# Optimization experiments

Hardware: AMD Instinct MI355X
Metric: run time of the kernel (lower is better)

Reference implementation:

```python
import math
import jax, jax.numpy as jnp
import numpy as np

# ---- static configuration (matches init_kwargs) ----
NM, NT, NF = 250000, 8000, 60000      # movable, terminals(fixed), filler
N = NM + NT + NF
XL = YL = ZL = 0.0
XH, YH, ZH = 512.0, 512.0, 8.0
BSX = BSY = BSZ = 1.0
NX = int(round((XH - XL) / BSX))
NY = int(round((YH - YL) / BSY))
NZ = int(round((ZH - ZL) / BSZ))
TD = 1.0                              # target density
PAD = 1
SQRT2 = 1.4142135623730951
BIN_VOL = BSX * BSY * BSZ


def _padding_mask():
    m = np.ones((NX, NY, NZ), dtype=bool)
    m[PAD:NX - PAD, PAD:NY - PAD, PAD:NZ - PAD] = False
    return jnp.asarray(m)


def _axis_overlap(p0, s, bl, bs, K, NB):
    """Overlap of segment [p0, p0+s] with K consecutive bins starting at floor bin.
    Returns bin indices [n,K], overlap lengths [n,K], validity mask [n,K]."""
    i0 = jnp.floor((p0 - bl) / bs).astype(jnp.int32)               # [n]
    k = i0[:, None] + jnp.arange(K, dtype=jnp.int32)               # [n,K]
    lo = bl + k.astype(p0.dtype) * bs                              # bin left edges
    ov = jnp.clip(jnp.minimum(p0[:, None] + s[:, None], lo + bs)
                  - jnp.maximum(p0[:, None], lo), 0.0)
    valid = (k >= 0) & (k < NB)
    return jnp.clip(k, 0, NB - 1), ov, valid


def _scatter_density(grid_flat, x0, y0, z0, sx, sy, sz, w, Kx, Ky, Kz):
    """Overlap-weighted scatter-add of boxes into the flat [NX*NY*NZ] density map."""
    kx, ox, vx = _axis_overlap(x0, sx, XL, BSX, Kx, NX)
    ky, oy, vy = _axis_overlap(y0, sy, YL, BSY, Ky, NY)
    kz, oz, vz = _axis_overlap(z0, sz, ZL, BSZ, Kz, NZ)
    val = (w[:, None, None, None]
           * ox[:, :, None, None] * oy[:, None, :, None] * oz[:, None, None, :])
    valid = vx[:, :, None, None] & vy[:, None, :, None] & vz[:, None, None, :]
    val = jnp.where(valid, val, 0.0)
    idx = (kx[:, :, None, None] * NY + ky[:, None, :, None]) * NZ + kz[:, None, None, :]
    return grid_flat.at[idx.reshape(-1)].add(val.reshape(-1))


def setup_inputs() -> dict:
    key = jax.random.key(0)
    k1, k2, k3, k4, k5, k6 = jax.random.split(key, 6)
    node_size_x = jax.random.uniform(k1, (N,), jnp.float32, 0.5, 1.0)
    node_size_y = jax.random.uniform(k2, (N,), jnp.float32, 0.5, 1.0)
    node_size_z = jax.random.uniform(k3, (N,), jnp.float32, 0.5, 1.0)
    px = jax.random.uniform(k4, (N,), jnp.float32, XL, XH - 1.0)
    py = jax.random.uniform(k5, (N,), jnp.float32, YL, YH - 1.0)
    pz = jax.random.uniform(k6, (N,), jnp.float32, ZL, ZH - 1.0)
    pos = jnp.concatenate([px, py, pz])  # flat x|y|z layout as in pos.view(numel)
    bin_center_x = XL + (jnp.arange(NX, dtype=jnp.float32) + 0.5) * BSX
    bin_center_y = YL + (jnp.arange(NY, dtype=jnp.float32) + 0.5) * BSY
    bin_center_z = ZL + (jnp.arange(NZ, dtype=jnp.float32) + 0.5) * BSZ
    sorted_node_map = jnp.arange(NM, dtype=jnp.int32)
    return {"pos": pos, "node_size_x": node_size_x, "node_size_y": node_size_y,
            "node_size_z": node_size_z, "bin_center_x": bin_center_x,
            "bin_center_y": bin_center_y, "bin_center_z": bin_center_z,
            "sorted_node_map": sorted_node_map}


def reference(pos, node_size_x, node_size_y, node_size_z,
              bin_center_x, bin_center_y, bin_center_z, sorted_node_map):
    px, py, pz = pos[:N], pos[N:2 * N], pos[2 * N:]

    # reset(): stretched (clamped) sizes, offsets, area-preserving ratio
    csx = jnp.maximum(node_size_x, BSX * SQRT2)
    csy = jnp.maximum(node_size_y, BSY * SQRT2)
    csz = jnp.maximum(node_size_z, BSZ * SQRT2)
    offx = (node_size_x - csx) * 0.5
    offy = (node_size_y - csy) * 0.5
    offz = (node_size_z - csz) * 0.5
    ratio = (node_size_x * node_size_y * node_size_z) / (csx * csy * csz)

    # ---- initial density map from fixed cells (terminals), actual sizes ----
    f0, f1 = NM, NM + NT
    Kfx = int(min(NX, math.ceil((float(jnp.max(node_size_x[f0:f1])) + BSX) / BSX)))
    Kfy = int(min(NY, math.ceil((float(jnp.max(node_size_y[f0:f1])) + BSY) / BSY)))
    Kfz = int(min(NZ, math.ceil((float(jnp.max(node_size_z[f0:f1])) + BSZ) / BSZ)))
    grid = jnp.zeros(NX * NY * NZ, dtype=jnp.float32)
    grid = _scatter_density(grid, px[f0:f1], py[f0:f1], pz[f0:f1],
                            node_size_x[f0:f1], node_size_y[f0:f1], node_size_z[f0:f1],
                            jnp.ones((NT,), jnp.float32), Kfx, Kfy, Kfz)
    grid = grid * TD  # initial_density_map.mul_(target_density)

    # ---- movable + filler cells: stretched sizes, offset, ratio weight ----
    mf = jnp.concatenate([jnp.arange(NM), jnp.arange(N - NF, N)])
    Kx = int(min(NX, math.ceil((float(jnp.max(node_size_x[mf])) + 2 * SQRT2 * BSX) / BSX)))
    Ky = int(min(NY, math.ceil((float(jnp.max(node_size_y[mf])) + 2 * SQRT2 * BSY) / BSY)))
    Kz = int(min(NZ, math.ceil((float(jnp.max(node_size_z[mf])) + 2 * SQRT2 * BSZ) / BSZ)))
    grid = _scatter_density(grid,
                            px[mf] + offx[mf], py[mf] + offy[mf], pz[mf] + offz[mf],
                            csx[mf], csy[mf], csz[mf], ratio[mf], Kx, Ky, Kz)

    density_map = grid.reshape(NX, NY, NZ)
    density_map = jnp.where(_padding_mask(), TD * BIN_VOL, density_map)

    density_cost = jnp.maximum(density_map - TD * BIN_VOL, 0.0).sum()[None]
    max_density = (density_map.max() / BIN_VOL)[None]
    return density_cost, max_density
```

## Files before the change

kernel.cpp:

```cpp
#include <hip/hip_runtime.h>

#define NMOV 250000
#define NTRM 8000
#define NTOT 318000
#define GNX 512
#define GNY 512
#define GNZ 8

static __device__ __forceinline__ float ovz(float pz, float pzh, int k) {
    float lo = (float)k;
    return fmaxf(fminf(pzh, lo + 1.0f) - fmaxf(pz, lo), 0.0f);
}
static __device__ __forceinline__ void node_box(
    int i, const float* __restrict__ pos,
    const float* __restrict__ nsx, const float* __restrict__ nsy, const float* __restrict__ nsz,
    float& px, float& py, float& pz, float& ex, float& ey, float& ez, float& w)
{
    px = pos[i]; py = pos[NTOT + i]; pz = pos[2 * NTOT + i];
    float sx = nsx[i], sy = nsy[i], sz = nsz[i];
    const float S2 = 1.4142135623730951f;
    bool terminal = (i >= NMOV) && (i < NMOV + NTRM);
    if (!terminal) {
        float cx = fmaxf(sx, S2), cy = fmaxf(sy, S2), cz = fmaxf(sz, S2);
        px += (sx - cx) * 0.5f;
        py += (sy - cy) * 0.5f;
        pz += (sz - cz) * 0.5f;
        w = (sx * sy * sz) / (cx * cy * cz);
        ex = cx; ey = cy; ez = cz;
    } else {
        ex = sx; ey = sy; ez = sz; w = 1.0f;
    }
}

#define NTIL8 4096
#define NSH8 8
#define CAPS8 40
#define TOTCAP 160

__global__ void fill32_kernel(const float* __restrict__ pos,
                              const float* __restrict__ nsx,
                              const float* __restrict__ nsy,
                              const float* __restrict__ nsz,
                              int* __restrict__ counts,
                              float4* __restrict__ bucket,
                              float* __restrict__ out) {
    int i = blockIdx.x * blockDim.x + threadIdx.x;
    if (i == 0) { out[0] = 0.0f; out[1] = 0.0f; }
    if (i >= NTOT) return;

    float pxl, pyl, pzl, ex, ey, ez, w;
    node_box(i, pos, nsx, nsy, nsz, pxl, pyl, pzl, ex, ey, ez, w);
    float pxh = pxl + ex, pyh = pyl + ey, pzh = pzl + ez;

    int iz0 = max((int)floorf(pzl), 0);
    float wza = w * ovz(pzl, pzh, iz0);
    float wzb = w * ovz(pzl, pzh, iz0 + 1);
    float wzc = (iz0 + 2 <= GNZ - 1) ? w * ovz(pzl, pzh, iz0 + 2) : 0.0f;

    float4 s0 = make_float4(pxl, pxh, pyl, pyh);
    float4 s1 = make_float4(wza, wzb, wzc, __int_as_float(iz0));

    int ix0 = max((int)floorf(pxl), 0);
    int ix1 = min((int)floorf(pxh), GNX - 1);
    int iy0 = max((int)floorf(pyl), 0);
    int iy1 = min((int)floorf(pyh), GNY - 1);
    int tx0 = ix0 >> 3, tx1 = ix1 >> 3;
    int ty0 = iy0 >> 3, ty1 = iy1 >> 3;
    int s = i & (NSH8 - 1);

    for (int tx = tx0; tx <= tx1; ++tx) {
        for (int ty = ty0; ty <= ty1; ++ty) {
            int cell = (((tx << 6) + ty) << 3) + s;
            int idx = atomicAdd(&counts[cell], 1);
            if (idx < CAPS8) {
                float4* sp = bucket + ((size_t)(cell * CAPS8 + idx) << 1);
                sp[0] = s0; sp[1] = s1;
            }
        }
    }
}

__launch_bounds__(256)
__global__ void accum32_kernel(const int* __restrict__ counts,
                               const float4* __restrict__ bucket,
                               float* __restrict__ out) {
    __shared__ float4 segQ[4][TOTCAP];
    __shared__ float4 segR[4][TOTCAP];
    __shared__ float scost[4], smx[4];

    int wid = threadIdx.x >> 6;
    int lane = threadIdx.x & 63;
    int t = (blockIdx.x << 2) + wid;
    int tx = t >> 6, ty = t & 63;
    int x = (tx << 3) + (lane >> 3);
    int y = (ty << 3) + (lane & 7);
    float Xf = (float)x, Yf = (float)y;
    float X1 = Xf + 1.0f, Y1 = Yf + 1.0f;

    float acc[GNZ];
    #pragma unroll
    for (int z = 0; z < GNZ; ++z) acc[z] = 0.0f;

    int cbase = t << 3;
    int c0 = min(counts[cbase + 0], CAPS8);
    int c1 = min(counts[cbase + 1], CAPS8);
    int c2 = min(counts[cbase + 2], CAPS8);
    int c3 = min(counts[cbase + 3], CAPS8);
    int c4 = min(counts[cbase + 4], CAPS8);
    int c5 = min(counts[cbase + 5], CAPS8);
    int c6 = min(counts[cbase + 6], CAPS8);
    int c7 = min(counts[cbase + 7], CAPS8);
    int o1 = c0, o2 = o1 + c1, o3 = o2 + c2, o4 = o3 + c3;
    int o5 = o4 + c4, o6 = o5 + c5, o7 = o6 + c6;
    int tot = o7 + c7;
    if (tot > TOTCAP) tot = TOTCAP;

    for (int g = lane; g < tot; g += 64) {
        int s = (g >= o1) + (g >= o2) + (g >= o3) + (g >= o4) +
                (g >= o5) + (g >= o6) + (g >= o7);
        int off = 0;
        off = (g >= o1) ? o1 : off;
        off = (g >= o2) ? o2 : off;
        off = (g >= o3) ? o3 : off;
        off = (g >= o4) ? o4 : off;
        off = (g >= o5) ? o5 : off;
        off = (g >= o6) ? o6 : off;
        off = (g >= o7) ? o7 : off;
        int idx = g - off;
        const float4* sp = bucket + ((size_t)((cbase + s) * CAPS8 + idx) << 1);
        segQ[wid][g] = sp[0];
        segR[wid][g] = sp[1];
    }

    for (int j = 0; j < tot; ++j) {
        float4 q = segQ[wid][j];
        float4 r = segR[wid][j];
        float ox = fmaxf(fminf(q.y, X1) - fmaxf(q.x, Xf), 0.0f);
        float oy = fmaxf(fminf(q.w, Y1) - fmaxf(q.z, Yf), 0.0f);
        float oxy = ox * oy;
        int iz0 = __builtin_amdgcn_readfirstlane(__float_as_int(r.w));
        switch (iz0) {
        case 0: acc[0]=fmaf(oxy,r.x,acc[0]); acc[1]=fmaf(oxy,r.y,acc[1]); acc[2]=fmaf(oxy,r.z,acc[2]); break;
        case 1: acc[1]=fmaf(oxy,r.x,acc[1]); acc[2]=fmaf(oxy,r.y,acc[2]); acc[3]=fmaf(oxy,r.z,acc[3]); break;
        case 2: acc[2]=fmaf(oxy,r.x,acc[2]); acc[3]=fmaf(oxy,r.y,acc[3]); acc[4]=fmaf(oxy,r.z,acc[4]); break;
        case 3: acc[3]=fmaf(oxy,r.x,acc[3]); acc[4]=fmaf(oxy,r.y,acc[4]); acc[5]=fmaf(oxy,r.z,acc[5]); break;
        case 4: acc[4]=fmaf(oxy,r.x,acc[4]); acc[5]=fmaf(oxy,r.y,acc[5]); acc[6]=fmaf(oxy,r.z,acc[6]); break;
        case 5: acc[5]=fmaf(oxy,r.x,acc[5]); acc[6]=fmaf(oxy,r.y,acc[6]); acc[7]=fmaf(oxy,r.z,acc[7]); break;
        default: acc[6]=fmaf(oxy,r.x,acc[6]); acc[7]=fmaf(oxy,r.y,acc[7]); break;
        }
    }

    float cost = 0.0f;
    float mx = 1.0f;
    if (x >= 1 && x <= GNX - 2 && y >= 1 && y <= GNY - 2) {
        #pragma unroll
        for (int z = 1; z <= GNZ - 2; ++z) {
            cost += fmaxf(acc[z] - 1.0f, 0.0f);
            mx = fmaxf(mx, acc[z]);
        }
    }
    #pragma unroll
    for (int off = 32; off >= 1; off >>= 1) {
        cost += __shfl_down(cost, off);
        mx = fmaxf(mx, __shfl_down(mx, off));
    }
    if (lane == 0) { scost[wid] = cost; smx[wid] = mx; }
    __syncthreads();
    if (threadIdx.x == 0) {
        float c = scost[0] + scost[1] + scost[2] + scost[3];
        float m = fmaxf(fmaxf(smx[0], smx[1]), fmaxf(smx[2], smx[3]));
        atomicAdd(&out[0], c);
        atomicMax((int*)&out[1], __float_as_int(m));
    }
}

__global__ void fill8s_kernel(const float* __restrict__ pos,
                              const float* __restrict__ nsx,
                              const float* __restrict__ nsy,
                              const float* __restrict__ nsz,
                              int* __restrict__ counts,
                              float4* __restrict__ bucket,
                              float* __restrict__ out) {
    int i = blockIdx.x * blockDim.x + threadIdx.x;
    if (i == 0) { out[0] = 0.0f; out[1] = 0.0f; }
    if (i >= NTOT) return;
    float pxl, pyl, pzl, ex, ey, ez, w;
    node_box(i, pos, nsx, nsy, nsz, pxl, pyl, pzl, ex, ey, ez, w);
    float pxh = pxl + ex, pyh = pyl + ey, pzh = pzl + ez;
    float4 q = make_float4(pxl, pxh, pyl, pyh);
    float4 a = make_float4(w * ovz(pzl, pzh, 0), w * ovz(pzl, pzh, 1),
                           w * ovz(pzl, pzh, 2), w * ovz(pzl, pzh, 3));
    float4 b = make_float4(w * ovz(pzl, pzh, 4), w * ovz(pzl, pzh, 5),
                           w * ovz(pzl, pzh, 6), w * ovz(pzl, pzh, 7));
    float4 pad = make_float4(0.0f, 0.0f, 0.0f, 0.0f);
    int ix0 = max((int)floorf(pxl), 0);
    int ix1 = min((int)floorf(pxh), GNX - 1);
    int iy0 = max((int)floorf(pyl), 0);
    int iy1 = min((int)floorf(pyh), GNY - 1);
    int tx0 = ix0 >> 3, tx1 = ix1 >> 3;
    int ty0 = iy0 >> 3, ty1 = iy1 >> 3;
    int s = i & (NSH8 - 1);
    for (int tx = tx0; tx <= tx1; ++tx) {
        for (int ty = ty0; ty <= ty1; ++ty) {
            int cell = (((tx << 6) + ty) << 3) + s;
            int idx = atomicAdd(&counts[cell], 1);
            if (idx < CAPS8) {
                float4* sp = bucket + ((size_t)(cell * CAPS8 + idx) << 2);
                sp[0] = q; sp[1] = a; sp[2] = b; sp[3] = pad;
            }
        }
    }
}

__launch_bounds__(256)
__global__ void accum8s_kernel(const int* __restrict__ counts,
                               const float4* __restrict__ bucket,
                               float* __restrict__ out) {
    __shared__ float4 seg[4][TOTCAP * 3];
    __shared__ float scost[4], smx[4];
    int wid = threadIdx.x >> 6;
    int lane = threadIdx.x & 63;
    int t = (blockIdx.x << 2) + wid;
    int tx = t >> 6, ty = t & 63;
    int x = (tx << 3) + (lane >> 3);
    int y = (ty << 3) + (lane & 7);
    float Xf = (float)x, Yf = (float)y;
    float acc[GNZ];
    #pragma unroll
    for (int z = 0; z < GNZ; ++z) acc[z] = 0.0f;
    int cbase = t << 3;
    int c0 = min(counts[cbase + 0], CAPS8);
    int c1 = min(counts[cbase + 1], CAPS8);
    int c2 = min(counts[cbase + 2], CAPS8);
    int c3 = min(counts[cbase + 3], CAPS8);
    int c4 = min(counts[cbase + 4], CAPS8);
    int c5 = min(counts[cbase + 5], CAPS8);
    int c6 = min(counts[cbase + 6], CAPS8);
    int c7 = min(counts[cbase + 7], CAPS8);
    int o1 = c0, o2 = o1 + c1, o3 = o2 + c2, o4 = o3 + c3;
    int o5 = o4 + c4, o6 = o5 + c5, o7 = o6 + c6;
    int tot = o7 + c7;
    if (tot > TOTCAP) tot = TOTCAP;
    for (int g = lane; g < tot; g += 64) {
        int s = (g >= o1) + (g >= o2) + (g >= o3) + (g >= o4) +
                (g >= o5) + (g >= o6) + (g >= o7);
        int off = 0;
        off = (g >= o1) ? o1 : off;
        off = (g >= o2) ? o2 : off;
        off = (g >= o3) ? o3 : off;
        off = (g >= o4) ? o4 : off;
        off = (g >= o5) ? o5 : off;
        off = (g >= o6) ? o6 : off;
        off = (g >= o7) ? o7 : off;
        int idx = g - off;
        const float4* sp = bucket + ((size_t)((cbase + s) * CAPS8 + idx) << 2);
        seg[wid][g * 3 + 0] = sp[0];
        seg[wid][g * 3 + 1] = sp[1];
        seg[wid][g * 3 + 2] = sp[2];
    }
    for (int j = 0; j < tot; ++j) {
        float4 q = seg[wid][3 * j];
        float ox = fmaxf(fminf(q.y, Xf + 1.0f) - fmaxf(q.x, Xf), 0.0f);
        float oy = fmaxf(fminf(q.w, Yf + 1.0f) - fmaxf(q.z, Yf), 0.0f);
        float oxy = ox * oy;
        float4 a = seg[wid][3 * j + 1];
        float4 b = seg[wid][3 * j + 2];
        acc[0] = fmaf(oxy, a.x, acc[0]);
        acc[1] = fmaf(oxy, a.y, acc[1]);
        acc[2] = fmaf(oxy, a.z, acc[2]);
        acc[3] = fmaf(oxy, a.w, acc[3]);
        acc[4] = fmaf(oxy, b.x, acc[4]);
        acc[5] = fmaf(oxy, b.y, acc[5]);
        acc[6] = fmaf(oxy, b.z, acc[6]);
        acc[7] = fmaf(oxy, b.w, acc[7]);
    }
    float cost = 0.0f;
    float mx = 1.0f;
    if (x >= 1 && x <= GNX - 2 && y >= 1 && y <= GNY - 2) {
        #pragma unroll
        for (int z = 1; z <= GNZ - 2; ++z) {
            cost += fmaxf(acc[z] - 1.0f, 0.0f);
            mx = fmaxf(mx, acc[z]);
        }
    }
    #pragma unroll
    for (int off = 32; off >= 1; off >>= 1) {
        cost += __shfl_down(cost, off);
        mx = fmaxf(mx, __shfl_down(mx, off));
    }
    if (lane == 0) { scost[wid] = cost; smx[wid] = mx; }
    __syncthreads();
    if (threadIdx.x == 0) {
        float c = scost[0] + scost[1] + scost[2] + scost[3];
        float m = fmaxf(fmaxf(smx[0], smx[1]), fmaxf(smx[2], smx[3]));
        atomicAdd(&out[0], c);
        atomicMax((int*)&out[1], __float_as_int(m));
    }
}

extern "C" void kernel_launch(void* const* d_in, const int* in_sizes, int n_in,
                              void* d_out, int out_size, void* d_ws, size_t ws_size,
                              hipStream_t stream) {
    const float* pos = (const float*)d_in[0];
    const float* nsx = (const float*)d_in[1];
    const float* nsy = (const float*)d_in[2];
    const float* nsz = (const float*)d_in[3];
    float* out = (float*)d_out;

    const size_t CNT = (size_t)NTIL8 * NSH8 * sizeof(int);
    const size_t NEED32 = CNT + (size_t)NTIL8 * NSH8 * CAPS8 * 32;
    const size_t NEED64 = CNT + (size_t)NTIL8 * NSH8 * CAPS8 * 64;

    if (ws_size >= NEED32) {
        int* counts = (int*)d_ws;
        float4* bucket = (float4*)((char*)d_ws + CNT);
        hipMemsetAsync(counts, 0, CNT, stream);
        fill32_kernel<<<(NTOT + 255) / 256, 256, 0, stream>>>(
            pos, nsx, nsy, nsz, counts, bucket, out);
        accum32_kernel<<<NTIL8 / 4, 256, 0, stream>>>(counts, bucket, out);
    } else if (ws_size >= NEED64) {
        int* counts = (int*)d_ws;
        float4* bucket = (float4*)((char*)d_ws + CNT);
        hipMemsetAsync(counts, 0, CNT, stream);
        fill8s_kernel<<<(NTOT + 255) / 256, 256, 0, stream>>>(
            pos, nsx, nsy, nsz, counts, bucket, out);
        accum8s_kernel<<<NTIL8 / 4, 256, 0, stream>>>(counts, bucket, out);
    }
}
```

Before: 137.9 us.

## Drop 32-byte bucket path; read 64-byte buckets directly from global in accumulate

Removes the compact 32-byte record path (fill32/accum32) and always uses the 64-byte record fill, which stores all eight z-weights. A new accumulate kernel skips the LDS staging and reads each bucket record straight from global memory, with uniform addresses across the wavefront (broadcast loads). It then applies 8 unconditional FMAs per record instead of a switch on iz0. This removes the shared-memory copy and the per-record branching, but doubles bucket write and read traffic and does 8 FMAs instead of 3.

```diff
diff --git a/kernel.cpp b/kernel.cpp
--- a/kernel.cpp
+++ b/kernel.cpp
@@ -35,144 +35,6 @@
 #define NTIL8 4096
 #define NSH8 8
 #define CAPS8 40
-#define TOTCAP 160
-
-__global__ void fill32_kernel(const float* __restrict__ pos,
-                              const float* __restrict__ nsx,
-                              const float* __restrict__ nsy,
-                              const float* __restrict__ nsz,
-                              int* __restrict__ counts,
-                              float4* __restrict__ bucket,
-                              float* __restrict__ out) {
-    int i = blockIdx.x * blockDim.x + threadIdx.x;
-    if (i == 0) { out[0] = 0.0f; out[1] = 0.0f; }
-    if (i >= NTOT) return;
-
-    float pxl, pyl, pzl, ex, ey, ez, w;
-    node_box(i, pos, nsx, nsy, nsz, pxl, pyl, pzl, ex, ey, ez, w);
-    float pxh = pxl + ex, pyh = pyl + ey, pzh = pzl + ez;
-
-    int iz0 = max((int)floorf(pzl), 0);
-    float wza = w * ovz(pzl, pzh, iz0);
-    float wzb = w * ovz(pzl, pzh, iz0 + 1);
-    float wzc = (iz0 + 2 <= GNZ - 1) ? w * ovz(pzl, pzh, iz0 + 2) : 0.0f;
-
-    float4 s0 = make_float4(pxl, pxh, pyl, pyh);
-    float4 s1 = make_float4(wza, wzb, wzc, __int_as_float(iz0));
-
-    int ix0 = max((int)floorf(pxl), 0);
-    int ix1 = min((int)floorf(pxh), GNX - 1);
-    int iy0 = max((int)floorf(pyl), 0);
-    int iy1 = min((int)floorf(pyh), GNY - 1);
-    int tx0 = ix0 >> 3, tx1 = ix1 >> 3;
-    int ty0 = iy0 >> 3, ty1 = iy1 >> 3;
-    int s = i & (NSH8 - 1);
-
-    for (int tx = tx0; tx <= tx1; ++tx) {
-        for (int ty = ty0; ty <= ty1; ++ty) {
-            int cell = (((tx << 6) + ty) << 3) + s;
-            int idx = atomicAdd(&counts[cell], 1);
-            if (idx < CAPS8) {
-                float4* sp = bucket + ((size_t)(cell * CAPS8 + idx) << 1);
-                sp[0] = s0; sp[1] = s1;
-            }
-        }
-    }
-}
-
-__launch_bounds__(256)
-__global__ void accum32_kernel(const int* __restrict__ counts,
-                               const float4* __restrict__ bucket,
-                               float* __restrict__ out) {
-    __shared__ float4 segQ[4][TOTCAP];
-    __shared__ float4 segR[4][TOTCAP];
-    __shared__ float scost[4], smx[4];
-
-    int wid = threadIdx.x >> 6;
-    int lane = threadIdx.x & 63;
-    int t = (blockIdx.x << 2) + wid;
-    int tx = t >> 6, ty = t & 63;
-    int x = (tx << 3) + (lane >> 3);
-    int y = (ty << 3) + (lane & 7);
-    float Xf = (float)x, Yf = (float)y;
-    float X1 = Xf + 1.0f, Y1 = Yf + 1.0f;
-
-    float acc[GNZ];
-    #pragma unroll
-    for (int z = 0; z < GNZ; ++z) acc[z] = 0.0f;
-
-    int cbase = t << 3;
-    int c0 = min(counts[cbase + 0], CAPS8);
-    int c1 = min(counts[cbase + 1], CAPS8);
-    int c2 = min(counts[cbase + 2], CAPS8);
-    int c3 = min(counts[cbase + 3], CAPS8);
-    int c4 = min(counts[cbase + 4], CAPS8);
-    int c5 = min(counts[cbase + 5], CAPS8);
-    int c6 = min(counts[cbase + 6], CAPS8);
-    int c7 = min(counts[cbase + 7], CAPS8);
-    int o1 = c0, o2 = o1 + c1, o3 = o2 + c2, o4 = o3 + c3;
-    int o5 = o4 + c4, o6 = o5 + c5, o7 = o6 + c6;
-    int tot = o7 + c7;
-    if (tot > TOTCAP) tot = TOTCAP;
-
-    for (int g = lane; g < tot; g += 64) {
-        int s = (g >= o1) + (g >= o2) + (g >= o3) + (g >= o4) +
-                (g >= o5) + (g >= o6) + (g >= o7);
-        int off = 0;
-        off = (g >= o1) ? o1 : off;
-        off = (g >= o2) ? o2 : off;
-        off = (g >= o3) ? o3 : off;
-        off = (g >= o4) ? o4 : off;
-        off = (g >= o5) ? o5 : off;
-        off = (g >= o6) ? o6 : off;
-        off = (g >= o7) ? o7 : off;
-        int idx = g - off;
-        const float4* sp = bucket + ((size_t)((cbase + s) * CAPS8 + idx) << 1);
-        segQ[wid][g] = sp[0];
-        segR[wid][g] = sp[1];
-    }
-
-    for (int j = 0; j < tot; ++j) {
-        float4 q = segQ[wid][j];
-        float4 r = segR[wid][j];
-        float ox = fmaxf(fminf(q.y, X1) - fmaxf(q.x, Xf), 0.0f);
-        float oy = fmaxf(fminf(q.w, Y1) - fmaxf(q.z, Yf), 0.0f);
-        float oxy = ox * oy;
-        int iz0 = __builtin_amdgcn_readfirstlane(__float_as_int(r.w));
-        switch (iz0) {
-        case 0: acc[0]=fmaf(oxy,r.x,acc[0]); acc[1]=fmaf(oxy,r.y,acc[1]); acc[2]=fmaf(oxy,r.z,acc[2]); break;
-        case 1: acc[1]=fmaf(oxy,r.x,acc[1]); acc[2]=fmaf(oxy,r.y,acc[2]); acc[3]=fmaf(oxy,r.z,acc[3]); break;
-        case 2: acc[2]=fmaf(oxy,r.x,acc[2]); acc[3]=fmaf(oxy,r.y,acc[3]); acc[4]=fmaf(oxy,r.z,acc[4]); break;
-        case 3: acc[3]=fmaf(oxy,r.x,acc[3]); acc[4]=fmaf(oxy,r.y,acc[4]); acc[5]=fmaf(oxy,r.z,acc[5]); break;
-        case 4: acc[4]=fmaf(oxy,r.x,acc[4]); acc[5]=fmaf(oxy,r.y,acc[5]); acc[6]=fmaf(oxy,r.z,acc[6]); break;
-        case 5: acc[5]=fmaf(oxy,r.x,acc[5]); acc[6]=fmaf(oxy,r.y,acc[6]); acc[7]=fmaf(oxy,r.z,acc[7]); break;
-        default: acc[6]=fmaf(oxy,r.x,acc[6]); acc[7]=fmaf(oxy,r.y,acc[7]); break;
-        }
-    }
-
-    float cost = 0.0f;
-    float mx = 1.0f;
-    if (x >= 1 && x <= GNX - 2 && y >= 1 && y <= GNY - 2) {
-        #pragma unroll
-        for (int z = 1; z <= GNZ - 2; ++z) {
-            cost += fmaxf(acc[z] - 1.0f, 0.0f);
-            mx = fmaxf(mx, acc[z]);
-        }
-    }
-    #pragma unroll
-    for (int off = 32; off >= 1; off >>= 1) {
-        cost += __shfl_down(cost, off);
-        mx = fmaxf(mx, __shfl_down(mx, off));
-    }
-    if (lane == 0) { scost[wid] = cost; smx[wid] = mx; }
-    __syncthreads();
-    if (threadIdx.x == 0) {
-        float c = scost[0] + scost[1] + scost[2] + scost[3];
-        float m = fmaxf(fmaxf(smx[0], smx[1]), fmaxf(smx[2], smx[3]));
-        atomicAdd(&out[0], c);
-        atomicMax((int*)&out[1], __float_as_int(m));
-    }
-}
 
 __global__ void fill8s_kernel(const float* __restrict__ pos,
                               const float* __restrict__ nsx,
@@ -184,15 +46,18 @@
     int i = blockIdx.x * blockDim.x + threadIdx.x;
     if (i == 0) { out[0] = 0.0f; out[1] = 0.0f; }
     if (i >= NTOT) return;
+
     float pxl, pyl, pzl, ex, ey, ez, w;
     node_box(i, pos, nsx, nsy, nsz, pxl, pyl, pzl, ex, ey, ez, w);
     float pxh = pxl + ex, pyh = pyl + ey, pzh = pzl + ez;
+
     float4 q = make_float4(pxl, pxh, pyl, pyh);
     float4 a = make_float4(w * ovz(pzl, pzh, 0), w * ovz(pzl, pzh, 1),
                            w * ovz(pzl, pzh, 2), w * ovz(pzl, pzh, 3));
     float4 b = make_float4(w * ovz(pzl, pzh, 4), w * ovz(pzl, pzh, 5),
                            w * ovz(pzl, pzh, 6), w * ovz(pzl, pzh, 7));
     float4 pad = make_float4(0.0f, 0.0f, 0.0f, 0.0f);
+
     int ix0 = max((int)floorf(pxl), 0);
     int ix1 = min((int)floorf(pxh), GNX - 1);
     int iy0 = max((int)floorf(pyl), 0);
@@ -200,6 +65,7 @@
     int tx0 = ix0 >> 3, tx1 = ix1 >> 3;
     int ty0 = iy0 >> 3, ty1 = iy1 >> 3;
     int s = i & (NSH8 - 1);
+
     for (int tx = tx0; tx <= tx1; ++tx) {
         for (int ty = ty0; ty <= ty1; ++ty) {
             int cell = (((tx << 6) + ty) << 3) + s;
@@ -211,6 +77,74 @@
         }
     }
 }
+
+__launch_bounds__(256)
+__global__ void accumg_kernel(const int* __restrict__ counts,
+                              const float4* __restrict__ bucket,
+                              float* __restrict__ out) {
+    __shared__ float scost[4], smx[4];
+
+    int wid = threadIdx.x >> 6;
+    int lane = threadIdx.x & 63;
+    int t = (blockIdx.x << 2) + wid;
+    int tx = t >> 6, ty = t & 63;
+    int x = (tx << 3) + (lane >> 3);
+    int y = (ty << 3) + (lane & 7);
+    float Xf = (float)x, Yf = (float)y;
+    float X1 = Xf + 1.0f, Y1 = Yf + 1.0f;
+
+    float acc[GNZ];
+    #pragma unroll
+    for (int z = 0; z < GNZ; ++z) acc[z] = 0.0f;
+
+    int cbase = t << 3;
+    for (int s = 0; s < NSH8; ++s) {
+        int n = min(counts[cbase + s], CAPS8);
+        const float4* sp = bucket + ((size_t)((cbase + s) * CAPS8) << 2);
+        #pragma unroll 4
+        for (int j = 0; j < n; ++j) {
+            float4 q = sp[(j << 2) + 0];
+            float4 a = sp[(j << 2) + 1];
+            float4 b = sp[(j << 2) + 2];
+            float ox = fmaxf(fminf(q.y, X1) - fmaxf(q.x, Xf), 0.0f);
+            float oy = fmaxf(fminf(q.w, Y1) - fmaxf(q.z, Yf), 0.0f);
+            float oxy = ox * oy;
+            acc[0] = fmaf(oxy, a.x, acc[0]);
+            acc[1] = fmaf(oxy, a.y, acc[1]);
+            acc[2] = fmaf(oxy, a.z, acc[2]);
+            acc[3] = fmaf(oxy, a.w, acc[3]);
+            acc[4] = fmaf(oxy, b.x, acc[4]);
+            acc[5] = fmaf(oxy, b.y, acc[5]);
+            acc[6] = fmaf(oxy, b.z, acc[6]);
+            acc[7] = fmaf(oxy, b.w, acc[7]);
+        }
+    }
+
+    float cost = 0.0f;
+    float mx = 1.0f;
+    if (x >= 1 && x <= GNX - 2 && y >= 1 && y <= GNY - 2) {
+        #pragma unroll
+        for (int z = 1; z <= GNZ - 2; ++z) {
+            cost += fmaxf(acc[z] - 1.0f, 0.0f);
+            mx = fmaxf(mx, acc[z]);
+        }
+    }
+    #pragma unroll
+    for (int off = 32; off >= 1; off >>= 1) {
+        cost += __shfl_down(cost, off);
+        mx = fmaxf(mx, __shfl_down(mx, off));
+    }
+    if (lane == 0) { scost[wid] = cost; smx[wid] = mx; }
+    __syncthreads();
+    if (threadIdx.x == 0) {
+        float c = scost[0] + scost[1] + scost[2] + scost[3];
+        float m = fmaxf(fmaxf(smx[0], smx[1]), fmaxf(smx[2], smx[3]));
+        atomicAdd(&out[0], c);
+        atomicMax((int*)&out[1], __float_as_int(m));
+    }
+}
+
+#define TOTCAP 160
 
 __launch_bounds__(256)
 __global__ void accum8s_kernel(const int* __restrict__ counts,
@@ -308,22 +242,15 @@
     float* out = (float*)d_out;
 
     const size_t CNT = (size_t)NTIL8 * NSH8 * sizeof(int);
-    const size_t NEED32 = CNT + (size_t)NTIL8 * NSH8 * CAPS8 * 32;
     const size_t NEED64 = CNT + (size_t)NTIL8 * NSH8 * CAPS8 * 64;
 
-    if (ws_size >= NEED32) {
-        int* counts = (int*)d_ws;
-        float4* bucket = (float4*)((char*)d_ws + CNT);
-        hipMemsetAsync(counts, 0, CNT, stream);
-        fill32_kernel<<<(NTOT + 255) / 256, 256, 0, stream>>>(
-            pos, nsx, nsy, nsz, counts, bucket, out);
-        accum32_kernel<<<NTIL8 / 4, 256, 0, stream>>>(counts, bucket, out);
-    } else if (ws_size >= NEED64) {
+    if (ws_size >= NEED64) {
         int* counts = (int*)d_ws;
         float4* bucket = (float4*)((char*)d_ws + CNT);
         hipMemsetAsync(counts, 0, CNT, stream);
         fill8s_kernel<<<(NTOT + 255) / 256, 256, 0, stream>>>(
             pos, nsx, nsy, nsz, counts, bucket, out);
-        accum8s_kernel<<<NTIL8 / 4, 256, 0, stream>>>(counts, bucket, out);
-    }
-}
+        accumg_kernel<<<NTIL8 / 4, 256, 0, stream>>>(counts, bucket, out);
+        (void)accum8s_kernel;
+    }
+}
```

New measurement: 159.9 us. 1.16x slower.
